# Kernel tuning notes

Measured on AMD Instinct MI355X. Metric: run time of the kernel, lower is better.

The kernel has to match this reference:

```python
import jax, jax.numpy as jnp
import numpy as np

B, S, D, H = 2, 2048, 1024, 16
d = D // H          # per-head dim (chunk along feature dim)
SEQ_LEN = 1024      # config.seq_len mask width
SCALE = float(np.sqrt(D))  # post-softmax divide by sqrt(model_dimension)
LN_EPS = 1e-5


def setup_inputs() -> dict:
    key = jax.random.key(0)
    ks = jax.random.split(key, 10)
    init = lambda k, shape: (jax.random.normal(k, shape, dtype=jnp.float32) * 0.02)
    return {
        "x": jax.random.normal(ks[0], (B, S, D), dtype=jnp.float32),
        "Wq": init(ks[1], (H, d, d)), "bq": jnp.zeros((H, d), jnp.float32),
        "Wk": init(ks[2], (H, d, d)), "bk": jnp.zeros((H, d), jnp.float32),
        "Wv": init(ks[3], (H, d, d)), "bv": jnp.zeros((H, d), jnp.float32),
        "Wo": init(ks[4], (D, D)),    "bo": jnp.zeros((D,), jnp.float32),
        "ln_g": jnp.ones((D,), jnp.float32),
        "ln_b": jnp.zeros((D,), jnp.float32),
    }


def reference(x, Wq, bq, Wk, bk, Wv, bv, Wo, bo, ln_g, ln_b):
    # chunk along feature dim == reshape D -> (H, d) since chunks are contiguous
    xh = x.reshape(B, S, H, d)                                  # [B,S,H,d]
    q = jnp.einsum('bshd,hde->bshe', xh, Wq) + bq               # [B,S,H,d]
    k = jnp.einsum('bshd,hde->bshe', xh, Wk) + bk
    v = jnp.einsum('bshd,hde->bshe', xh, Wv) + bv
    scores = jnp.einsum('bshd,bthd->bhst', q, k)                # [B,H,S,S]
    # custom mask: last query row, last SEQ_LEN key columns -> -inf
    scores = scores.at[:, :, -1, -SEQ_LEN:].set(-jnp.inf)
    attn = jax.nn.softmax(scores, axis=-1) / SCALE              # post-softmax scale
    o = jnp.einsum('bhst,bthd->bshd', attn, v).reshape(B, S, D) # concat heads
    proj = jnp.einsum('bsd,de->bse', o, Wo) + bo                # output projection
    y = x + proj                                                 # residual
    mu = jnp.mean(y, axis=-1, keepdims=True)
    var = jnp.mean(jnp.square(y - mu), axis=-1, keepdims=True)
    return (y - mu) * jax.lax.rsqrt(var + LN_EPS) * ln_g + ln_b
```

## Files before the change

### kernel.cpp

```cpp
#include <hip/hip_runtime.h>
#include <math.h>

#define B 2
#define S 2048
#define D 1024
#define H 16
#define HD 64
#define LN_EPS 1e-5f
#define LOG2E 1.44269504f
#define KSPLIT 2
#define NTS (S / 64 / KSPLIT)
#define NBD_ELEMS (B * S * D)
#define BHS_ELEMS (B * H * S)

typedef __bf16 bf16x8 __attribute__((ext_vector_type(8)));
typedef float f32x4 __attribute__((ext_vector_type(4)));

#if defined(__has_builtin)
#if __has_builtin(__builtin_amdgcn_exp2f)
#define EXP2(x) __builtin_amdgcn_exp2f(x)
#endif
#endif
#ifndef EXP2
#define EXP2(x) __expf((x) * 0.6931471805599453f)
#endif

__device__ __forceinline__ ushort f2bf(float f) {
    uint u = __float_as_uint(f);
    u += 0x7FFFu + ((u >> 16) & 1u);
    return (ushort)(u >> 16);
}

__device__ __forceinline__ bf16x8 ldfrag(const char* base, int row, int cbyte) {
    int a = row * 128 + (cbyte ^ ((row & 7) << 4));
    union { uint4 u; bf16x8 v; } c;
    c.u = *(const uint4*)(base + a);
    return c.v;
}

__device__ __forceinline__ uint comb2(uint a, uint b, float inv) {
    float lo = (__uint_as_float(a << 16) + __uint_as_float(b << 16)) * inv;
    float hi = (__uint_as_float(a & 0xFFFF0000u) + __uint_as_float(b & 0xFFFF0000u)) * inv;
    return (uint)f2bf(lo) | ((uint)f2bf(hi) << 16);
}

__global__ __launch_bounds__(256) void cvt_kernel(
        const float* __restrict__ Wo,
        const float* __restrict__ Wq, const float* __restrict__ Wk,
        const float* __restrict__ Wv,
        ushort* __restrict__ wt, ushort* __restrict__ wqt,
        ushort* __restrict__ wkt, ushort* __restrict__ wvt) {
    __shared__ float t[64][65];
    int tid = threadIdx.x;
    if (blockIdx.y < 16) {
        int r0 = blockIdx.y * 64, c0 = blockIdx.x * 64;
#pragma unroll
        for (int it = 0; it < 16; ++it) {
            int idx = tid + 256 * it;
            int row = idx >> 6, col = idx & 63;
            t[row][col] = Wo[(size_t)(r0 + row) * D + c0 + col];
        }
        __syncthreads();
#pragma unroll
        for (int it = 0; it < 16; ++it) {
            int idx = tid + 256 * it;
            int nrow = idx >> 6, kcol = idx & 63;
            wt[(size_t)(c0 + nrow) * D + r0 + kcol] = f2bf(t[kcol][nrow]);
        }
    } else {
        int h = blockIdx.x, which = blockIdx.y - 16;
        const float* W = (which == 0) ? Wq : (which == 1) ? Wk : Wv;
        ushort* outp = (which == 0) ? wqt : (which == 1) ? wkt : wvt;
        const float* Wh = W + h * HD * HD;
        ushort* oh = outp + h * HD * HD;
#pragma unroll
        for (int it = 0; it < 16; ++it) {
            int idx = tid + 256 * it;
            t[idx >> 6][idx & 63] = Wh[idx];
        }
        __syncthreads();
#pragma unroll
        for (int it = 0; it < 16; ++it) {
            int idx = tid + 256 * it;
            int e = idx >> 6, dd = idx & 63;
            oh[idx] = f2bf(t[dd][e]);
        }
    }
}

__global__ __launch_bounds__(256) void qkv_kernel(
        const float* __restrict__ x,
        const ushort* __restrict__ wqt, const ushort* __restrict__ wkt,
        const ushort* __restrict__ wvt,
        const float* __restrict__ bq, const float* __restrict__ bk,
        const float* __restrict__ bv,
        ushort* __restrict__ qh, ushort* __restrict__ kh, ushort* __restrict__ vth) {
    __shared__ char xt[16384];
    const int tid = threadIdx.x;
    const int w = tid >> 6, l = tid & 63;
    const int lg = l >> 4, lr = l & 15;
    const int h = blockIdx.y;
    const size_t row0 = (size_t)blockIdx.x * 128;
    const int b = (int)(row0 >> 11);
    const int s0 = (int)(row0 & (S - 1));
    const size_t hb = (size_t)b * H + h;

#pragma unroll
    for (int it = 0; it < 4; ++it) {
        int c = tid + 256 * it;
        int row = c >> 3, sub = c & 7;
        const float* src = x + (row0 + row) * D + h * HD + 8 * sub;
        float4 f0 = *(const float4*)src;
        float4 f1 = *(const float4*)(src + 4);
        uint2 lo = make_uint2((uint)f2bf(f0.x) | ((uint)f2bf(f0.y) << 16),
                              (uint)f2bf(f0.z) | ((uint)f2bf(f0.w) << 16));
        uint2 hi = make_uint2((uint)f2bf(f1.x) | ((uint)f2bf(f1.y) << 16),
                              (uint)f2bf(f1.z) | ((uint)f2bf(f1.w) << 16));
        int p0 = 64 * (sub >> 2) + 32 * (sub & 1) + 8 * ((sub >> 1) & 1);
        int sz = (row & 7) << 4;
        char* dst = xt + row * 128;
        *(uint2*)(dst + (p0 ^ sz)) = lo;
        *(uint2*)(dst + ((p0 + 16) ^ sz)) = hi;
    }
    __syncthreads();

    bf16x8 xa[2][2];
#pragma unroll
    for (int fm = 0; fm < 2; ++fm)
#pragma unroll
        for (int ks = 0; ks < 2; ++ks)
            xa[fm][ks] = ldfrag(xt, 32 * w + 16 * fm + lr, 64 * ks + 16 * lg);

#pragma unroll
    for (int tsel = 0; tsel < 3; ++tsel) {
        const ushort* wsrc = (tsel == 0) ? wqt : (tsel == 1) ? wkt : wvt;
        const float* bsrc = (tsel == 0) ? bq : (tsel == 1) ? bk : bv;
        bf16x8 wf[4][2];
#pragma unroll
        for (int fn = 0; fn < 4; ++fn) {
            const char* wp = (const char*)(wsrc + ((size_t)h * HD + 16 * fn + lr) * HD);
#pragma unroll
            for (int ks = 0; ks < 2; ++ks) {
                uint2 a = *(const uint2*)(wp + 64 * ks + 8 * lg);
                uint2 c2 = *(const uint2*)(wp + 64 * ks + 8 * lg + 32);
                union { uint4 u; bf16x8 v; } cc;
                cc.u = make_uint4(a.x, a.y, c2.x, c2.y);
                wf[fn][ks] = cc.v;
            }
        }
        f32x4 acc[2][4];
#pragma unroll
        for (int fm = 0; fm < 2; ++fm)
#pragma unroll
            for (int fn = 0; fn < 4; ++fn)
#pragma unroll
                for (int r = 0; r < 4; ++r) acc[fm][fn][r] = 0.f;
#pragma unroll
        for (int fm = 0; fm < 2; ++fm)
#pragma unroll
            for (int fn = 0; fn < 4; ++fn)
#pragma unroll
                for (int ks = 0; ks < 2; ++ks)
                    acc[fm][fn] = __builtin_amdgcn_mfma_f32_16x16x32_bf16(
                        xa[fm][ks], wf[fn][ks], acc[fm][fn], 0, 0, 0);
        if (tsel == 0) {
#pragma unroll
            for (int fn = 0; fn < 4; ++fn) {
                float bias = bsrc[h * HD + 16 * fn + lr];
#pragma unroll
                for (int fm = 0; fm < 2; ++fm)
#pragma unroll
                    for (int r = 0; r < 4; ++r) {
                        int srow = s0 + 32 * w + 16 * fm + 4 * lg + r;
                        qh[(hb * S + srow) * HD + 16 * fn + lr] =
                            f2bf((acc[fm][fn][r] + bias) * LOG2E);
                    }
            }
        } else if (tsel == 1) {
#pragma unroll
            for (int fn = 0; fn < 4; ++fn) {
                float bias = bsrc[h * HD + 16 * fn + lr];
#pragma unroll
                for (int fm = 0; fm < 2; ++fm)
#pragma unroll
                    for (int r = 0; r < 4; ++r) {
                        int srow = s0 + 32 * w + 16 * fm + 4 * lg + r;
                        kh[(hb * S + srow) * HD + 16 * fn + lr] =
                            f2bf(acc[fm][fn][r] + bias);
                    }
            }
        } else {
#pragma unroll
            for (int fn = 0; fn < 4; ++fn) {
                float bias = bsrc[h * HD + 16 * fn + lr];
                int e = 16 * fn + lr;
#pragma unroll
                for (int fm = 0; fm < 2; ++fm) {
                    uint2 pk;
                    pk.x = (uint)f2bf(acc[fm][fn][0] + bias) |
                           ((uint)f2bf(acc[fm][fn][1] + bias) << 16);
                    pk.y = (uint)f2bf(acc[fm][fn][2] + bias) |
                           ((uint)f2bf(acc[fm][fn][3] + bias) << 16);
                    *(uint2*)(vth + (hb * HD + e) * S + s0 + 32 * w + 16 * fm + 4 * lg) = pk;
                }
            }
        }
    }
}

__global__ __launch_bounds__(512) void attn_kernel(
        const ushort* __restrict__ qh, const ushort* __restrict__ kh,
        const ushort* __restrict__ vth, ushort* __restrict__ ou,
        float* __restrict__ ls) {
    __shared__ char kt[3][8192];
    __shared__ char vt[3][8192];
    const int tid = threadIdx.x;
    const int w = tid >> 6, l = tid & 63;
    const int lg = l >> 4, lr = l & 15;
    const int flat = blockIdx.x + 8 * (blockIdx.y + 2 * blockIdx.z);
    const int xc = flat & 7, sl = flat >> 3;
    const int g = xc + 8 * (sl & 7);
    const int qi = sl >> 3;
    const int ksp = g >> 5;
    const int h = g & (H - 1), b = (g >> 4) & 1;
    const int q0 = qi * 256 + 32 * w;
    const size_t bh = (size_t)b * H + h;
    const ushort* qbase = qh + bh * S * HD;
    const ushort* kbase = kh + bh * S * HD;
    const ushort* vbase = vth + bh * HD * S;

    const int r0s = tid >> 3, ssub = tid & 7;
    const int sp0 = 64 * (ssub >> 2) + 32 * (ssub & 1) + 8 * ((ssub >> 1) & 1);
    const int ssz = (r0s & 7) << 4;

    bf16x8 qf[2][2];
#pragma unroll
    for (int fn = 0; fn < 2; ++fn) {
        const char* qp = (const char*)(qbase + (size_t)(q0 + 16 * fn + lr) * HD);
#pragma unroll
        for (int ks = 0; ks < 2; ++ks) {
            uint2 xlo = *(const uint2*)(qp + 64 * ks + 8 * lg);
            uint2 xhi = *(const uint2*)(qp + 64 * ks + 8 * lg + 32);
            union { uint4 u; bf16x8 v; } c;
            c.u = make_uint4(xlo.x, xlo.y, xhi.x, xhi.y);
            qf[fn][ks] = c.v;
        }
    }

    f32x4 acc[2][4];
#pragma unroll
    for (int fn = 0; fn < 2; ++fn)
#pragma unroll
        for (int n0 = 0; n0 < 4; ++n0)
#pragma unroll
            for (int r = 0; r < 4; ++r) acc[fn][n0][r] = 0.f;
    f32x4 accs[2];
#pragma unroll
    for (int fn = 0; fn < 2; ++fn)
#pragma unroll
        for (int r = 0; r < 4; ++r) accs[fn][r] = 0.f;
    const f32x4 z4 = {0.f, 0.f, 0.f, 0.f};
    bf16x8 onef;
#pragma unroll
    for (int j = 0; j < 8; ++j) onef[j] = (__bf16)1.0f;
    const bool lastq = (q0 + 32 == S) && (lr == 15);

    {
        const int kv0 = ksp * NTS * 64;
        uint4 kd = *(const uint4*)(kbase + (size_t)(kv0 + r0s) * HD + 8 * ssub);
        uint4 vd = *(const uint4*)(vbase + (size_t)r0s * S + kv0 + 8 * ssub);
        char* kr = kt[0] + r0s * 128;
        char* vr = vt[0] + r0s * 128;
        *(uint2*)(kr + (sp0 ^ ssz)) = make_uint2(kd.x, kd.y);
        *(uint2*)(kr + ((sp0 + 16) ^ ssz)) = make_uint2(kd.z, kd.w);
        *(uint2*)(vr + (sp0 ^ ssz)) = make_uint2(vd.x, vd.y);
        *(uint2*)(vr + ((sp0 + 16) ^ ssz)) = make_uint2(vd.z, vd.w);
    }
    __syncthreads();

    int cur = 0;
    for (int t = 0; t < NTS; ++t) {
        const int kv0 = (ksp * NTS + t) * 64;
        int nxt = cur + 1; if (nxt == 3) nxt = 0;
        uint4 kd2, vd2;
        if (t + 1 < NTS) {
            kd2 = *(const uint4*)(kbase + (size_t)(kv0 + 64 + r0s) * HD + 8 * ssub);
            vd2 = *(const uint4*)(vbase + (size_t)r0s * S + kv0 + 64 + 8 * ssub);
        }

        const char* ktb = kt[cur];
        const char* vtb = vt[cur];
        __builtin_amdgcn_s_setprio(1);
        f32x4 s[4][2];
#pragma unroll
        for (int fm = 0; fm < 4; ++fm) {
            bf16x8 k0 = ldfrag(ktb, fm * 16 + lr, 16 * lg);
            bf16x8 k1 = ldfrag(ktb, fm * 16 + lr, 64 + 16 * lg);
#pragma unroll
            for (int fn = 0; fn < 2; ++fn) {
                s[fm][fn] = __builtin_amdgcn_mfma_f32_16x16x32_bf16(k0, qf[fn][0], z4, 0, 0, 0);
                s[fm][fn] = __builtin_amdgcn_mfma_f32_16x16x32_bf16(k1, qf[fn][1], s[fm][fn], 0, 0, 0);
            }
        }
        if (lastq && kv0 >= S - 1024) {
#pragma unroll
            for (int fm = 0; fm < 4; ++fm)
#pragma unroll
                for (int r = 0; r < 4; ++r) s[fm][1][r] = -INFINITY;
        }

        bf16x8 pa[2][2];
#pragma unroll
        for (int fn = 0; fn < 2; ++fn)
#pragma unroll
            for (int ks = 0; ks < 2; ++ks)
#pragma unroll
                for (int j = 0; j < 8; ++j)
                    pa[fn][ks][j] = (__bf16)EXP2(s[(j >> 2) + 2 * ks][fn][j & 3]);
#pragma unroll
        for (int fn = 0; fn < 2; ++fn) {
            accs[fn] = __builtin_amdgcn_mfma_f32_16x16x32_bf16(pa[fn][0], onef, accs[fn], 0, 0, 0);
            accs[fn] = __builtin_amdgcn_mfma_f32_16x16x32_bf16(pa[fn][1], onef, accs[fn], 0, 0, 0);
        }
#pragma unroll
        for (int n0 = 0; n0 < 4; ++n0) {
            bf16x8 v0 = ldfrag(vtb, n0 * 16 + lr, 16 * lg);
            bf16x8 v1 = ldfrag(vtb, n0 * 16 + lr, 64 + 16 * lg);
#pragma unroll
            for (int fn = 0; fn < 2; ++fn) {
                acc[fn][n0] = __builtin_amdgcn_mfma_f32_16x16x32_bf16(pa[fn][0], v0, acc[fn][n0], 0, 0, 0);
                acc[fn][n0] = __builtin_amdgcn_mfma_f32_16x16x32_bf16(pa[fn][1], v1, acc[fn][n0], 0, 0, 0);
            }
        }
        __builtin_amdgcn_s_setprio(0);

        if (t + 1 < NTS) {
            char* kr = kt[nxt] + r0s * 128;
            char* vr = vt[nxt] + r0s * 128;
            *(uint2*)(kr + (sp0 ^ ssz)) = make_uint2(kd2.x, kd2.y);
            *(uint2*)(kr + ((sp0 + 16) ^ ssz)) = make_uint2(kd2.z, kd2.w);
            *(uint2*)(vr + (sp0 ^ ssz)) = make_uint2(vd2.x, vd2.y);
            *(uint2*)(vr + ((sp0 + 16) ^ ssz)) = make_uint2(vd2.z, vd2.w);
            __syncthreads();
        }
        cur = nxt;
    }

#pragma unroll
    for (int fn = 0; fn < 2; ++fn)
#pragma unroll
        for (int r = 0; r < 4; ++r) {
            int qrow = q0 + 16 * fn + 4 * lg + r;
            ushort* op = ou + (((size_t)ksp * B + b) * S + qrow) * D + h * HD;
#pragma unroll
            for (int n0 = 0; n0 < 4; ++n0)
                op[n0 * 16 + lr] = f2bf(acc[fn][n0][r]);
            if (lr == 0)
                ls[(((size_t)ksp * B + b) * H + h) * S + qrow] = accs[fn][r];
        }
}

__global__ __launch_bounds__(256) void proj_gemm_kernel(
        const ushort* __restrict__ ou, const float* __restrict__ ls,
        const ushort* __restrict__ wt,
        const float* __restrict__ x, const float* __restrict__ bo,
        float* __restrict__ yws) {
    __shared__ char at[3][8192];
    __shared__ char btl[3][16384];
    const int tid = threadIdx.x;
    const int w = tid >> 6, l = tid & 63;
    const int lg = l >> 4, lr = l & 15;
    const int wr = w >> 1, wc = w & 1;
    const int flat = blockIdx.x + 8 * blockIdx.y;
    const int xc = flat & 7, sl = flat >> 3;
    const int m0 = (xc + 8 * (sl & 7)) * 64;
    const int n0 = (sl >> 3) * 128;

    const ushort* srcA[2];
    const float* lsp[2];
    int offA1[2], offA2[2];
#pragma unroll
    for (int it = 0; it < 2; ++it) {
        int c = tid + 256 * it;
        int row = c >> 3, sub = c & 7;
        int r = m0 + row;
        srcA[it] = ou + (size_t)r * D + 8 * sub;
        int b = r >> 11, s = r & (S - 1);
        lsp[it] = ls + (size_t)b * H * S + s;
        int p0 = 64 * (sub >> 2) + 32 * (sub & 1) + 8 * ((sub >> 1) & 1);
        int sz = (row & 7) << 4;
        offA1[it] = row * 128 + (p0 ^ sz);
        offA2[it] = row * 128 + ((p0 + 16) ^ sz);
    }
    const ushort* srcB[4];
    int offB1[4], offB2[4];
#pragma unroll
    for (int it = 0; it < 4; ++it) {
        int c = tid + 256 * it;
        int row = c >> 3, sub = c & 7;
        srcB[it] = wt + (size_t)(n0 + row) * D + 8 * sub;
        int p0 = 64 * (sub >> 2) + 32 * (sub & 1) + 8 * ((sub >> 1) & 1);
        int sz = (row & 7) << 4;
        offB1[it] = row * 128 + (p0 ^ sz);
        offB2[it] = row * 128 + ((p0 + 16) ^ sz);
    }

    f32x4 acc[2][4];
#pragma unroll
    for (int fm = 0; fm < 2; ++fm)
#pragma unroll
        for (int fn = 0; fn < 4; ++fn)
#pragma unroll
            for (int r = 0; r < 4; ++r) acc[fm][fn][r] = 0.f;

    uint4 pa0[2], pa1[2], pb[4];
    float pl0[2], pl1[2];

    auto LOADT = [&](int t) {
#pragma unroll
        for (int it = 0; it < 2; ++it) {
            pa0[it] = *(const uint4*)(srcA[it] + (size_t)t * 64);
            pa1[it] = *(const uint4*)(srcA[it] + (size_t)NBD_ELEMS + (size_t)t * 64);
            pl0[it] = lsp[it][(size_t)t * S];
            pl1[it] = lsp[it][(size_t)BHS_ELEMS + (size_t)t * S];
        }
#pragma unroll
        for (int it = 0; it < 4; ++it)
            pb[it] = *(const uint4*)(srcB[it] + (size_t)t * 64);
    };
    auto STORET = [&](int buf) {
#pragma unroll
        for (int it = 0; it < 2; ++it) {
            float inv = 1.0f / ((pl0[it] + pl1[it]) * 32.0f);
            uint cx = comb2(pa0[it].x, pa1[it].x, inv);
            uint cy = comb2(pa0[it].y, pa1[it].y, inv);
            uint cz = comb2(pa0[it].z, pa1[it].z, inv);
            uint cw = comb2(pa0[it].w, pa1[it].w, inv);
            *(uint2*)(at[buf] + offA1[it]) = make_uint2(cx, cy);
            *(uint2*)(at[buf] + offA2[it]) = make_uint2(cz, cw);
        }
#pragma unroll
        for (int it = 0; it < 4; ++it) {
            *(uint2*)(btl[buf] + offB1[it]) = make_uint2(pb[it].x, pb[it].y);
            *(uint2*)(btl[buf] + offB2[it]) = make_uint2(pb[it].z, pb[it].w);
        }
    };

    LOADT(0);
    STORET(0);
    __syncthreads();

    int cur = 0;
    for (int t = 0; t < D / 64; ++t) {
        int nxt = cur + 1; if (nxt == 3) nxt = 0;
        if (t + 1 < D / 64) LOADT(t + 1);

        bf16x8 af[2][2], bfr[4][2];
#pragma unroll
        for (int fm = 0; fm < 2; ++fm)
#pragma unroll
            for (int ks = 0; ks < 2; ++ks)
                af[fm][ks] = ldfrag(at[cur], 32 * wr + 16 * fm + lr, 64 * ks + 16 * lg);
#pragma unroll
        for (int fn = 0; fn < 4; ++fn)
#pragma unroll
            for (int ks = 0; ks < 2; ++ks)
                bfr[fn][ks] = ldfrag(btl[cur], 64 * wc + 16 * fn + lr, 64 * ks + 16 * lg);
#pragma unroll
        for (int fm = 0; fm < 2; ++fm)
#pragma unroll
            for (int fn = 0; fn < 4; ++fn)
#pragma unroll
                for (int ks = 0; ks < 2; ++ks)
                    acc[fm][fn] = __builtin_amdgcn_mfma_f32_16x16x32_bf16(
                        af[fm][ks], bfr[fn][ks], acc[fm][fn], 0, 0, 0);

        if (t + 1 < D / 64) {
            STORET(nxt);
            __syncthreads();
        }
        cur = nxt;
    }

#pragma unroll
    for (int fm = 0; fm < 2; ++fm)
#pragma unroll
        for (int fn = 0; fn < 4; ++fn) {
            int col = n0 + 64 * wc + 16 * fn + lr;
            float bov = bo[col];
#pragma unroll
            for (int r = 0; r < 4; ++r) {
                int rowg = m0 + 32 * wr + 16 * fm + 4 * lg + r;
                size_t off = (size_t)rowg * D + col;
                yws[off] = acc[fm][fn][r] + x[off] + bov;
            }
        }
}

__global__ __launch_bounds__(256) void ln_kernel(
        const float* __restrict__ yws, const float* __restrict__ g,
        const float* __restrict__ bb, float* __restrict__ out) {
    __shared__ float rs[4], rq[4];
    int tid = threadIdx.x;
    size_t row = blockIdx.x;
    float4 yv = *(const float4*)(yws + row * D + tid * 4);
    float s = yv.x + yv.y + yv.z + yv.w;
    float q = yv.x * yv.x + yv.y * yv.y + yv.z * yv.z + yv.w * yv.w;
    for (int off = 32; off > 0; off >>= 1) {
        s += __shfl_down(s, off, 64);
        q += __shfl_down(q, off, 64);
    }
    if ((tid & 63) == 0) { rs[tid >> 6] = s; rq[tid >> 6] = q; }
    __syncthreads();
    float sum = rs[0] + rs[1] + rs[2] + rs[3];
    float sq  = rq[0] + rq[1] + rq[2] + rq[3];
    float mean = sum * (1.0f / D);
    float var  = sq * (1.0f / D) - mean * mean;
    float rstd = rsqrtf(var + LN_EPS);
    float4 gv = *(const float4*)(g + tid * 4);
    float4 bv = *(const float4*)(bb + tid * 4);
    float4 ov;
    ov.x = (yv.x - mean) * rstd * gv.x + bv.x;
    ov.y = (yv.y - mean) * rstd * gv.y + bv.y;
    ov.z = (yv.z - mean) * rstd * gv.z + bv.z;
    ov.w = (yv.w - mean) * rstd * gv.w + bv.w;
    *(float4*)(out + row * D + tid * 4) = ov;
}

extern "C" void kernel_launch(void* const* d_in, const int* in_sizes, int n_in,
                              void* d_out, int out_size, void* d_ws, size_t ws_size,
                              hipStream_t stream) {
    const float* x  = (const float*)d_in[0];
    const float* Wq = (const float*)d_in[1];
    const float* bq = (const float*)d_in[2];
    const float* Wk = (const float*)d_in[3];
    const float* bk = (const float*)d_in[4];
    const float* Wv = (const float*)d_in[5];
    const float* bv = (const float*)d_in[6];
    const float* Wo = (const float*)d_in[7];
    const float* bo = (const float*)d_in[8];
    const float* g  = (const float*)d_in[9];
    const float* bb = (const float*)d_in[10];
    float* out = (float*)d_out;

    const size_t NBD = (size_t)B * S * D;
    ushort* qh  = (ushort*)d_ws;
    ushort* kh  = qh + NBD;
    ushort* vth = kh + NBD;
    ushort* wt  = vth + NBD;
    ushort* wqt = wt + (size_t)D * D;
    ushort* wkt = wqt + H * HD * HD;
    ushort* wvt = wkt + H * HD * HD;
    ushort* ou  = wvt + H * HD * HD;
    float*  ls  = (float*)(ou + (size_t)KSPLIT * NBD);
    float*  yws = (float*)d_ws;

    cvt_kernel<<<dim3(16, 19), 256, 0, stream>>>(Wo, Wq, Wk, Wv, wt, wqt, wkt, wvt);
    qkv_kernel<<<dim3((B * S) / 128, H), 256, 0, stream>>>(
        x, wqt, wkt, wvt, bq, bk, bv, qh, kh, vth);
    attn_kernel<<<dim3(S / 256, KSPLIT, H * B), 512, 0, stream>>>(qh, kh, vth, ou, ls);
    proj_gemm_kernel<<<dim3(D / 128, (B * S) / 64), 256, 0, stream>>>(ou, ls, wt, x, bo, yws);
    ln_kernel<<<dim3(B * S), 256, 0, stream>>>(yws, g, bb, out);
}
```

Before: 93.68 us.

## Give each attention wave 64 query rows with 256-thread blocks

```diff
diff --git a/kernel.cpp b/kernel.cpp
--- a/kernel.cpp
+++ b/kernel.cpp
@@ -208,7 +208,7 @@
     }
 }
 
-__global__ __launch_bounds__(512) void attn_kernel(
+__global__ __launch_bounds__(256) void attn_kernel(
         const ushort* __restrict__ qh, const ushort* __restrict__ kh,
         const ushort* __restrict__ vth, ushort* __restrict__ ou,
         float* __restrict__ ls) {
@@ -223,7 +223,7 @@
     const int qi = sl >> 3;
     const int ksp = g >> 5;
     const int h = g & (H - 1), b = (g >> 4) & 1;
-    const int q0 = qi * 256 + 32 * w;
+    const int q0 = qi * 256 + 64 * w;
     const size_t bh = (size_t)b * H + h;
     const ushort* qbase = qh + bh * S * HD;
     const ushort* kbase = kh + bh * S * HD;
@@ -233,9 +233,9 @@
     const int sp0 = 64 * (ssub >> 2) + 32 * (ssub & 1) + 8 * ((ssub >> 1) & 1);
     const int ssz = (r0s & 7) << 4;
 
-    bf16x8 qf[2][2];
-#pragma unroll
-    for (int fn = 0; fn < 2; ++fn) {
+    bf16x8 qf[4][2];
+#pragma unroll
+    for (int fn = 0; fn < 4; ++fn) {
         const char* qp = (const char*)(qbase + (size_t)(q0 + 16 * fn + lr) * HD);
 #pragma unroll
         for (int ks = 0; ks < 2; ++ks) {
@@ -247,34 +247,38 @@
         }
     }
 
-    f32x4 acc[2][4];
-#pragma unroll
-    for (int fn = 0; fn < 2; ++fn)
+    f32x4 acc[4][4];
+#pragma unroll
+    for (int fn = 0; fn < 4; ++fn)
 #pragma unroll
         for (int n0 = 0; n0 < 4; ++n0)
 #pragma unroll
             for (int r = 0; r < 4; ++r) acc[fn][n0][r] = 0.f;
-    f32x4 accs[2];
-#pragma unroll
-    for (int fn = 0; fn < 2; ++fn)
+    f32x4 accs[4];
+#pragma unroll
+    for (int fn = 0; fn < 4; ++fn)
 #pragma unroll
         for (int r = 0; r < 4; ++r) accs[fn][r] = 0.f;
     const f32x4 z4 = {0.f, 0.f, 0.f, 0.f};
     bf16x8 onef;
 #pragma unroll
     for (int j = 0; j < 8; ++j) onef[j] = (__bf16)1.0f;
-    const bool lastq = (q0 + 32 == S) && (lr == 15);
+    const bool lastq = (q0 + 64 == S) && (lr == 15);
 
     {
         const int kv0 = ksp * NTS * 64;
-        uint4 kd = *(const uint4*)(kbase + (size_t)(kv0 + r0s) * HD + 8 * ssub);
-        uint4 vd = *(const uint4*)(vbase + (size_t)r0s * S + kv0 + 8 * ssub);
-        char* kr = kt[0] + r0s * 128;
-        char* vr = vt[0] + r0s * 128;
-        *(uint2*)(kr + (sp0 ^ ssz)) = make_uint2(kd.x, kd.y);
-        *(uint2*)(kr + ((sp0 + 16) ^ ssz)) = make_uint2(kd.z, kd.w);
-        *(uint2*)(vr + (sp0 ^ ssz)) = make_uint2(vd.x, vd.y);
-        *(uint2*)(vr + ((sp0 + 16) ^ ssz)) = make_uint2(vd.z, vd.w);
+#pragma unroll
+        for (int it = 0; it < 2; ++it) {
+            int row = r0s + 32 * it;
+            uint4 kd = *(const uint4*)(kbase + (size_t)(kv0 + row) * HD + 8 * ssub);
+            uint4 vd = *(const uint4*)(vbase + (size_t)row * S + kv0 + 8 * ssub);
+            char* kr = kt[0] + row * 128;
+            char* vr = vt[0] + row * 128;
+            *(uint2*)(kr + (sp0 ^ ssz)) = make_uint2(kd.x, kd.y);
+            *(uint2*)(kr + ((sp0 + 16) ^ ssz)) = make_uint2(kd.z, kd.w);
+            *(uint2*)(vr + (sp0 ^ ssz)) = make_uint2(vd.x, vd.y);
+            *(uint2*)(vr + ((sp0 + 16) ^ ssz)) = make_uint2(vd.z, vd.w);
+        }
     }
     __syncthreads();
 
@@ -282,43 +286,48 @@
     for (int t = 0; t < NTS; ++t) {
         const int kv0 = (ksp * NTS + t) * 64;
         int nxt = cur + 1; if (nxt == 3) nxt = 0;
-        uint4 kd2, vd2;
+        uint4 kd2[2], vd2[2];
         if (t + 1 < NTS) {
-            kd2 = *(const uint4*)(kbase + (size_t)(kv0 + 64 + r0s) * HD + 8 * ssub);
-            vd2 = *(const uint4*)(vbase + (size_t)r0s * S + kv0 + 64 + 8 * ssub);
+#pragma unroll
+            for (int it = 0; it < 2; ++it) {
+                int row = r0s + 32 * it;
+                kd2[it] = *(const uint4*)(kbase + (size_t)(kv0 + 64 + row) * HD + 8 * ssub);
+                vd2[it] = *(const uint4*)(vbase + (size_t)row * S + kv0 + 64 + 8 * ssub);
+            }
         }
 
         const char* ktb = kt[cur];
         const char* vtb = vt[cur];
         __builtin_amdgcn_s_setprio(1);
-        f32x4 s[4][2];
-#pragma unroll
-        for (int fm = 0; fm < 4; ++fm) {
-            bf16x8 k0 = ldfrag(ktb, fm * 16 + lr, 16 * lg);
-            bf16x8 k1 = ldfrag(ktb, fm * 16 + lr, 64 + 16 * lg);
-#pragma unroll
-            for (int fn = 0; fn < 2; ++fn) {
-                s[fm][fn] = __builtin_amdgcn_mfma_f32_16x16x32_bf16(k0, qf[fn][0], z4, 0, 0, 0);
-                s[fm][fn] = __builtin_amdgcn_mfma_f32_16x16x32_bf16(k1, qf[fn][1], s[fm][fn], 0, 0, 0);
-            }
-        }
-        if (lastq && kv0 >= S - 1024) {
-#pragma unroll
-            for (int fm = 0; fm < 4; ++fm)
-#pragma unroll
-                for (int r = 0; r < 4; ++r) s[fm][1][r] = -INFINITY;
-        }
-
-        bf16x8 pa[2][2];
-#pragma unroll
-        for (int fn = 0; fn < 2; ++fn)
-#pragma unroll
-            for (int ks = 0; ks < 2; ++ks)
+        bf16x8 pa[4][2];
+#pragma unroll
+        for (int half = 0; half < 2; ++half) {
+            f32x4 s2[2][4];
+#pragma unroll
+            for (int fm2 = 0; fm2 < 2; ++fm2) {
+                int fm = 2 * half + fm2;
+                bf16x8 k0 = ldfrag(ktb, fm * 16 + lr, 16 * lg);
+                bf16x8 k1 = ldfrag(ktb, fm * 16 + lr, 64 + 16 * lg);
+#pragma unroll
+                for (int fn = 0; fn < 4; ++fn) {
+                    s2[fm2][fn] = __builtin_amdgcn_mfma_f32_16x16x32_bf16(k0, qf[fn][0], z4, 0, 0, 0);
+                    s2[fm2][fn] = __builtin_amdgcn_mfma_f32_16x16x32_bf16(k1, qf[fn][1], s2[fm2][fn], 0, 0, 0);
+                }
+            }
+            if (lastq && kv0 >= S - 1024) {
+#pragma unroll
+                for (int fm2 = 0; fm2 < 2; ++fm2)
+#pragma unroll
+                    for (int r = 0; r < 4; ++r) s2[fm2][3][r] = -INFINITY;
+            }
+#pragma unroll
+            for (int fn = 0; fn < 4; ++fn)
 #pragma unroll
                 for (int j = 0; j < 8; ++j)
-                    pa[fn][ks][j] = (__bf16)EXP2(s[(j >> 2) + 2 * ks][fn][j & 3]);
-#pragma unroll
-        for (int fn = 0; fn < 2; ++fn) {
+                    pa[fn][half][j] = (__bf16)EXP2(s2[j >> 2][fn][j & 3]);
+        }
+#pragma unroll
+        for (int fn = 0; fn < 4; ++fn) {
             accs[fn] = __builtin_amdgcn_mfma_f32_16x16x32_bf16(pa[fn][0], onef, accs[fn], 0, 0, 0);
             accs[fn] = __builtin_amdgcn_mfma_f32_16x16x32_bf16(pa[fn][1], onef, accs[fn], 0, 0, 0);
         }
@@ -327,7 +336,7 @@
             bf16x8 v0 = ldfrag(vtb, n0 * 16 + lr, 16 * lg);
             bf16x8 v1 = ldfrag(vtb, n0 * 16 + lr, 64 + 16 * lg);
 #pragma unroll
-            for (int fn = 0; fn < 2; ++fn) {
+            for (int fn = 0; fn < 4; ++fn) {
                 acc[fn][n0] = __builtin_amdgcn_mfma_f32_16x16x32_bf16(pa[fn][0], v0, acc[fn][n0], 0, 0, 0);
                 acc[fn][n0] = __builtin_amdgcn_mfma_f32_16x16x32_bf16(pa[fn][1], v1, acc[fn][n0], 0, 0, 0);
             }
@@ -335,19 +344,23 @@
         __builtin_amdgcn_s_setprio(0);
 
         if (t + 1 < NTS) {
-            char* kr = kt[nxt] + r0s * 128;
-            char* vr = vt[nxt] + r0s * 128;
-            *(uint2*)(kr + (sp0 ^ ssz)) = make_uint2(kd2.x, kd2.y);
-            *(uint2*)(kr + ((sp0 + 16) ^ ssz)) = make_uint2(kd2.z, kd2.w);
-            *(uint2*)(vr + (sp0 ^ ssz)) = make_uint2(vd2.x, vd2.y);
-            *(uint2*)(vr + ((sp0 + 16) ^ ssz)) = make_uint2(vd2.z, vd2.w);
+#pragma unroll
+            for (int it = 0; it < 2; ++it) {
+                int row = r0s + 32 * it;
+                char* kr = kt[nxt] + row * 128;
+                char* vr = vt[nxt] + row * 128;
+                *(uint2*)(kr + (sp0 ^ ssz)) = make_uint2(kd2[it].x, kd2[it].y);
+                *(uint2*)(kr + ((sp0 + 16) ^ ssz)) = make_uint2(kd2[it].z, kd2[it].w);
+                *(uint2*)(vr + (sp0 ^ ssz)) = make_uint2(vd2[it].x, vd2[it].y);
+                *(uint2*)(vr + ((sp0 + 16) ^ ssz)) = make_uint2(vd2[it].z, vd2[it].w);
+            }
             __syncthreads();
         }
         cur = nxt;
     }
 
 #pragma unroll
-    for (int fn = 0; fn < 2; ++fn)
+    for (int fn = 0; fn < 4; ++fn)
 #pragma unroll
         for (int r = 0; r < 4; ++r) {
             int qrow = q0 + 16 * fn + 4 * lg + r;
@@ -558,7 +571,7 @@
     cvt_kernel<<<dim3(16, 19), 256, 0, stream>>>(Wo, Wq, Wk, Wv, wt, wqt, wkt, wvt);
     qkv_kernel<<<dim3((B * S) / 128, H), 256, 0, stream>>>(
         x, wqt, wkt, wvt, bq, bk, bv, qh, kh, vth);
-    attn_kernel<<<dim3(S / 256, KSPLIT, H * B), 512, 0, stream>>>(qh, kh, vth, ou, ls);
+    attn_kernel<<<dim3(S / 256, KSPLIT, H * B), 256, 0, stream>>>(qh, kh, vth, ou, ls);
     proj_gemm_kernel<<<dim3(D / 128, (B * S) / 64), 256, 0, stream>>>(ou, ls, wt, x, bo, yws);
     ln_kernel<<<dim3(B * S), 256, 0, stream>>>(yws, g, bb, out);
 }
```

Result: slower. 98.34 us (+5.0%).
